# Kernel optimization log

Hardware: AMD Instinct MI355X
Metric: run time of the kernel (lower is better)

The kernel has to match this reference:

```python
import jax, jax.numpy as jnp
import numpy as np

K_NEIGHBORS = 3  # self.K in DSVDD


def setup_inputs() -> dict:
    key = jax.random.key(0)
    k1, k2 = jax.random.split(key)
    B, N, C = 16, 3136, 112   # batch, h*w patches, descriptor channels
    M = 3136                  # memory-bank size
    phi_p = jax.random.normal(k1, (B, N, C), dtype=jnp.float32)
    C_bank = jax.random.normal(k2, (C, M), dtype=jnp.float32)
    return {"phi_p": phi_p, "C_bank": C_bank, "h": 56}


def reference(phi_p, C_bank, h):
    # squared distances via ||phi||^2 + ||c||^2 - 2 phi.c  -> (B, N, M)
    features = jnp.sum(phi_p * phi_p, axis=2, keepdims=True)        # (B, N, 1)
    centers = jnp.sum(C_bank * C_bank, axis=0, keepdims=True)       # (1, M)
    f_c = 2.0 * jnp.einsum('bnc,cm->bnm', phi_p, C_bank)            # (B, N, M)
    dist = jnp.sqrt(features + centers - f_c)                        # (B, N, M)
    # K smallest distances (ascending, like torch.topk(largest=False))
    neg_topk, _ = jax.lax.top_k(-dist, K_NEIGHBORS)                  # (B, N, K)
    dist_k = -neg_topk
    # softmin over K, take weight of the nearest neighbor times its distance
    softmin0 = jax.nn.softmax(-dist_k, axis=-1)[:, :, 0]             # (B, N)
    score = softmin0 * dist_k[:, :, 0]                               # (B, N)
    B, N = score.shape
    w = N // h
    return score.reshape(B, 1, h, w)  # b c h w with c=1
```

## Files before the change

### kernel.cpp

```cpp
#include <hip/hip_runtime.h>
#include <stdint.h>


typedef short s16x8 __attribute__((ext_vector_type(8)));
typedef float fx4 __attribute__((ext_vector_type(4)));

#define M_TOT 3136
#define CC 112
#define NROWS 50176
#define N_TILES_TOT 50

__device__ __forceinline__ unsigned short f2bf(float x) {
  unsigned u = __float_as_uint(x);
  u += 0x7fffu + ((u >> 16) & 1u);
  return (unsigned short)(u >> 16);
}

#define INSERT3(T0, T1, T2, V)                                  \
  do {                                                          \
    const float _a0 = (T0), _a1 = (T1), _v = (V);               \
    (T0) = fmaxf(_a0, _v);                                      \
    (T1) = __builtin_amdgcn_fmed3f(_a0, _a1, _v);               \
    (T2) = __builtin_amdgcn_fmed3f(_a1, (T2), _v);              \
  } while (0)

__global__ __launch_bounds__(256) void dsvdd_prep(const float* __restrict__ Cb,
                                                  unsigned char* __restrict__ CT2) {
  const int tile = blockIdx.x;
  __shared__ float partial[256];
  __shared__ float c2s[64];
  const int tm = threadIdx.x & 63;
  const int seg = threadIdx.x >> 6;
  const int m = tile * 64 + tm;
  float ss = 0.f;
  if (m < M_TOT) {
    for (int k = seg * 28; k < seg * 28 + 28; ++k) {
      const float x = Cb[(size_t)k * M_TOT + m];
      ss += x * x;
    }
  }
  partial[threadIdx.x] = ss;
  __syncthreads();
  if (seg == 0) {
    const float c2 = partial[tm] + partial[64 + tm] + partial[128 + tm] + partial[192 + tm];
    c2s[tm] = (m < M_TOT) ? (-0.125f * c2) : -2500.0f;
  }
  __syncthreads();
#pragma unroll
  for (int it = 0; it < 4; ++it) {
    const int s = it * 256 + threadIdx.x;
    const int f = s >> 8;
    const int ks = (s >> 6) & 3;
    const int l = s & 63;
    const int mloc = f * 16 + (l & 15);
    const int mm = tile * 64 + mloc;
    const bool mv = (mm < M_TOT);
    const int k0 = ks * 32 + (l >> 4) * 8;
    float v[8];
#pragma unroll
    for (int j = 0; j < 8; ++j) {
      const int k = k0 + j;
      float x = 0.f;
      if (k < CC) x = mv ? Cb[(size_t)k * M_TOT + mm] : 0.f;
      else if (k < 116) x = c2s[mloc];
      v[j] = x;
    }
    uint4 pk;
    pk.x = (unsigned)f2bf(v[0]) | ((unsigned)f2bf(v[1]) << 16);
    pk.y = (unsigned)f2bf(v[2]) | ((unsigned)f2bf(v[3]) << 16);
    pk.z = (unsigned)f2bf(v[4]) | ((unsigned)f2bf(v[5]) << 16);
    pk.w = (unsigned)f2bf(v[6]) | ((unsigned)f2bf(v[7]) << 16);
    *(uint4*)(CT2 + (size_t)tile * 16384 + (size_t)s * 16) = pk;
  }
}

__global__ __launch_bounds__(256, 2) void dsvdd_stage1(const float* __restrict__ phi,
                                                       const unsigned char* __restrict__ CT2,
                                                       float* __restrict__ part,
                                                       float* __restrict__ featg, int nT) {
  __shared__ float mg[128][8];

  const int t = threadIdx.x;
  const int lane = t & 63;
  const int w = t >> 6;
  const int g = w >> 1;
  const int h = w & 1;
  const int cq = lane & 15;
  const int kq = lane >> 4;
  const int c = blockIdx.y;
  const int tile0 = c * nT;
  const long rowBase = (long)blockIdx.x * 128;
  const bool needF = (c == 0);

  s16x8 bg[4][4];
  float ssr[4];
#pragma unroll
  for (int pf = 0; pf < 4; ++pf) {
    ssr[pf] = 0.f;
    const float* rp = phi + (size_t)(rowBase + g * 64 + pf * 16 + cq) * CC;
#pragma unroll
    for (int ks = 0; ks < 4; ++ks) {
      const int k0 = ks * 32 + kq * 8;
      s16x8 v;
      if (k0 <= 104) {
        const float4 a = *(const float4*)(rp + k0);
        const float4 b = *(const float4*)(rp + k0 + 4);
        if (needF) {
          ssr[pf] += a.x * a.x + a.y * a.y + a.z * a.z + a.w * a.w;
          ssr[pf] += b.x * b.x + b.y * b.y + b.z * b.z + b.w * b.w;
        }
        v[0] = (short)f2bf(a.x); v[1] = (short)f2bf(a.y);
        v[2] = (short)f2bf(a.z); v[3] = (short)f2bf(a.w);
        v[4] = (short)f2bf(b.x); v[5] = (short)f2bf(b.y);
        v[6] = (short)f2bf(b.z); v[7] = (short)f2bf(b.w);
      } else if (k0 == 112) {
        v[0] = v[1] = v[2] = v[3] = (short)0x3f80;
        v[4] = v[5] = v[6] = v[7] = 0;
      } else {
        v = (s16x8)0;
      }
      bg[ks][pf] = v;
    }
    if (needF) {
      ssr[pf] += __shfl_xor(ssr[pf], 16);
      ssr[pf] += __shfl_xor(ssr[pf], 32);
    }
  }
  if (needF && kq == 0) {
#pragma unroll
    for (int pf = 0; pf < 4; ++pf)
      featg[rowBase + g * 64 + pf * 16 + cq] = ssr[pf];
  }

  float t0[4], t1[4], t2[4];
#pragma unroll
  for (int pf = 0; pf < 4; ++pf) t0[pf] = t1[pf] = t2[pf] = -3.0e38f;

  const unsigned char* ap = CT2 + (size_t)(h * 2) * 4096 + (size_t)lane * 16;
  s16x8 afA[8], afB[8];

#define LOADAF(DST, TIDX)                                                     \
  do {                                                                        \
    const unsigned char* _p = ap + (size_t)(TIDX)*16384;                      \
    _Pragma("unroll") for (int mf = 0; mf < 2; ++mf)                          \
        _Pragma("unroll") for (int ks = 0; ks < 4; ++ks)                      \
            DST[mf * 4 + ks] = *(const s16x8*)(_p + mf * 4096 + ks * 1024);   \
  } while (0)

#define COMPUTE(SRC)                                                          \
  do {                                                                        \
    const fx4 _zz = {0.f, 0.f, 0.f, 0.f};                                     \
    _Pragma("unroll") for (int mf = 0; mf < 2; ++mf) {                        \
      fx4 acc[4];                                                             \
      _Pragma("unroll") for (int ks = 0; ks < 4; ++ks)                        \
          _Pragma("unroll") for (int pf = 0; pf < 4; ++pf)                    \
              acc[pf] = __builtin_amdgcn_mfma_f32_16x16x32_bf16(              \
                  SRC[mf * 4 + ks], bg[ks][pf], (ks == 0) ? _zz : acc[pf],    \
                  0, 0, 0);                                                   \
      _Pragma("unroll") for (int pf = 0; pf < 4; ++pf)                        \
          _Pragma("unroll") for (int rg = 0; rg < 4; ++rg)                    \
              INSERT3(t0[pf], t1[pf], t2[pf], acc[pf][rg]);                   \
    }                                                                         \
  } while (0)

  LOADAF(afA, tile0);
  int tt = 0;
  while (tt + 2 < nT) {
    LOADAF(afB, tile0 + tt + 1);
    COMPUTE(afA);
    LOADAF(afA, tile0 + tt + 2);
    COMPUTE(afB);
    tt += 2;
  }
  if (tt + 1 < nT) {
    LOADAF(afB, tile0 + tt + 1);
    COMPUTE(afA);
    COMPUTE(afB);
  } else {
    COMPUTE(afA);
  }
#undef LOADAF
#undef COMPUTE

#pragma unroll
  for (int pf = 0; pf < 4; ++pf) {
#pragma unroll
    for (int off = 16; off < 64; off <<= 1) {
      const float b0 = __shfl_xor(t0[pf], off);
      const float b1 = __shfl_xor(t1[pf], off);
      const float b2 = __shfl_xor(t2[pf], off);
      INSERT3(t0[pf], t1[pf], t2[pf], b0);
      INSERT3(t0[pf], t1[pf], t2[pf], b1);
      INSERT3(t0[pf], t1[pf], t2[pf], b2);
    }
  }
  if (kq == 0) {
#pragma unroll
    for (int pf = 0; pf < 4; ++pf) {
      const int row = g * 64 + pf * 16 + cq;
      mg[row][h * 3 + 0] = t0[pf];
      mg[row][h * 3 + 1] = t1[pf];
      mg[row][h * 3 + 2] = t2[pf];
    }
  }
  __syncthreads();
  if (t < 128) {
    float s0 = mg[t][0], s1 = mg[t][1], s2 = mg[t][2];
    INSERT3(s0, s1, s2, mg[t][3]);
    INSERT3(s0, s1, s2, mg[t][4]);
    INSERT3(s0, s1, s2, mg[t][5]);
    float* dst = part + ((size_t)c * NROWS + rowBase + t) * 3;
    dst[0] = s0; dst[1] = s1; dst[2] = s2;
  }
}

__global__ __launch_bounds__(256) void dsvdd_stage2(const float* __restrict__ part,
                                                    const float* __restrict__ featg,
                                                    float* __restrict__ out, int S) {
  const int row = blockIdx.x * 256 + threadIdx.x;
  if (row >= NROWS) return;
  float s0 = -3.0e38f, s1 = -3.0e38f, s2 = -3.0e38f;
  for (int c = 0; c < S; ++c) {
    const float* p = part + ((size_t)c * NROWS + row) * 3;
    INSERT3(s0, s1, s2, p[0]);
    INSERT3(s0, s1, s2, p[1]);
    INSERT3(s0, s1, s2, p[2]);
  }
  const float feat = featg[row];
  const float d0 = sqrtf(fmaxf(feat - 2.f * s0, 0.f));
  const float d1 = sqrtf(fmaxf(feat - 2.f * s1, 0.f));
  const float d2 = sqrtf(fmaxf(feat - 2.f * s2, 0.f));
  const float w0 = 1.0f / (1.0f + __expf(d0 - d1) + __expf(d0 - d2));
  out[row] = w0 * d0;
}

extern "C" void kernel_launch(void* const* d_in, const int* in_sizes, int n_in,
                              void* d_out, int out_size, void* d_ws, size_t ws_size,
                              hipStream_t stream) {
  (void)in_sizes; (void)n_in; (void)out_size;
  const float* phi = (const float*)d_in[0];
  const float* Cb = (const float*)d_in[1];
  float* out = (float*)d_out;
  unsigned char* CT2 = (unsigned char*)d_ws;
  float* featg = (float*)((unsigned char*)d_ws + 819200);
  float* partp = (float*)((unsigned char*)d_ws + 819200 + 200704);
  const size_t base = 819200 + 200704;
  int S = 1;
  if (ws_size >= base + (size_t)5 * NROWS * 12) S = 5;
  else if (ws_size >= base + (size_t)2 * NROWS * 12) S = 2;
  const int nT = N_TILES_TOT / S;
  dsvdd_prep<<<50, 256, 0, stream>>>(Cb, CT2);
  dsvdd_stage1<<<dim3(392, S), 256, 0, stream>>>(phi, CT2, partp, featg, nT);
  dsvdd_stage2<<<196, 256, 0, stream>>>(partp, featg, out, S);
}
```

Measured before the change: 64.28 us.

## Stage phi rows through shared memory and raise occupancy target to three blocks

Each block now loads its 128 phi rows cooperatively with contiguous per-thread reads, converts them to bf16 once, and writes them into a 32KB shared buffer in MFMA fragment order. Waves then read their B fragments from LDS. Before, each wave converted its own rows from global memory and both wave halves duplicated that work. Launch bounds are also raised to 3 blocks per CU, which cuts the register budget and may cause spills given the large fragment arrays.

```diff
diff --git a/kernel.cpp b/kernel.cpp
--- a/kernel.cpp
+++ b/kernel.cpp
@@ -74,11 +74,12 @@
   }
 }
 
-__global__ __launch_bounds__(256, 2) void dsvdd_stage1(const float* __restrict__ phi,
+__global__ __launch_bounds__(256, 3) void dsvdd_stage1(const float* __restrict__ phi,
                                                        const unsigned char* __restrict__ CT2,
                                                        float* __restrict__ part,
                                                        float* __restrict__ featg, int nT) {
-  __shared__ float mg[128][8];
+  __shared__ __align__(16) unsigned char phiF[32768];
+  float(*const mg)[8] = (float(*)[8])phiF;
 
   const int t = threadIdx.x;
   const int lane = t & 63;
@@ -92,45 +93,47 @@
   const long rowBase = (long)blockIdx.x * 128;
   const bool needF = (c == 0);
 
+  {
+    const int r = t >> 1;
+    const int h2 = t & 1;
+    const float* src = phi + (size_t)(rowBase + r) * CC + h2 * 56;
+    unsigned char* const base = phiF + (((r >> 4) * 4) * 1024);
+    const int pcq = r & 15;
+    float ss = 0.f;
+#pragma unroll
+    for (int j = 0; j < 7; ++j) {
+      const int k0 = h2 * 56 + j * 8;
+      const int ks = k0 >> 5;
+      const int kqw = (k0 >> 3) & 3;
+      const float4 a = *(const float4*)(src + j * 8);
+      const float4 b = *(const float4*)(src + j * 8 + 4);
+      ss += a.x * a.x + a.y * a.y + a.z * a.z + a.w * a.w;
+      ss += b.x * b.x + b.y * b.y + b.z * b.z + b.w * b.w;
+      uint4 pk;
+      pk.x = (unsigned)f2bf(a.x) | ((unsigned)f2bf(a.y) << 16);
+      pk.y = (unsigned)f2bf(a.z) | ((unsigned)f2bf(a.w) << 16);
+      pk.z = (unsigned)f2bf(b.x) | ((unsigned)f2bf(b.y) << 16);
+      pk.w = (unsigned)f2bf(b.z) | ((unsigned)f2bf(b.w) << 16);
+      *(uint4*)(base + ks * 1024 + (kqw * 16 + pcq) * 16) = pk;
+    }
+    {
+      uint4 pk;
+      if (h2 == 0) { pk.x = 0x3f803f80u; pk.y = 0x3f803f80u; pk.z = 0u; pk.w = 0u; }
+      else { pk.x = pk.y = pk.z = pk.w = 0u; }
+      *(uint4*)(base + 3 * 1024 + ((2 + h2) * 16 + pcq) * 16) = pk;
+    }
+    ss += __shfl_xor(ss, 1);
+    if (needF && h2 == 0) featg[rowBase + r] = ss;
+  }
+  __syncthreads();
+
   s16x8 bg[4][4];
-  float ssr[4];
-#pragma unroll
-  for (int pf = 0; pf < 4; ++pf) {
-    ssr[pf] = 0.f;
-    const float* rp = phi + (size_t)(rowBase + g * 64 + pf * 16 + cq) * CC;
-#pragma unroll
-    for (int ks = 0; ks < 4; ++ks) {
-      const int k0 = ks * 32 + kq * 8;
-      s16x8 v;
-      if (k0 <= 104) {
-        const float4 a = *(const float4*)(rp + k0);
-        const float4 b = *(const float4*)(rp + k0 + 4);
-        if (needF) {
-          ssr[pf] += a.x * a.x + a.y * a.y + a.z * a.z + a.w * a.w;
-          ssr[pf] += b.x * b.x + b.y * b.y + b.z * b.z + b.w * b.w;
-        }
-        v[0] = (short)f2bf(a.x); v[1] = (short)f2bf(a.y);
-        v[2] = (short)f2bf(a.z); v[3] = (short)f2bf(a.w);
-        v[4] = (short)f2bf(b.x); v[5] = (short)f2bf(b.y);
-        v[6] = (short)f2bf(b.z); v[7] = (short)f2bf(b.w);
-      } else if (k0 == 112) {
-        v[0] = v[1] = v[2] = v[3] = (short)0x3f80;
-        v[4] = v[5] = v[6] = v[7] = 0;
-      } else {
-        v = (s16x8)0;
-      }
-      bg[ks][pf] = v;
-    }
-    if (needF) {
-      ssr[pf] += __shfl_xor(ssr[pf], 16);
-      ssr[pf] += __shfl_xor(ssr[pf], 32);
-    }
-  }
-  if (needF && kq == 0) {
+#pragma unroll
+  for (int ks = 0; ks < 4; ++ks)
 #pragma unroll
     for (int pf = 0; pf < 4; ++pf)
-      featg[rowBase + g * 64 + pf * 16 + cq] = ssr[pf];
-  }
+      bg[ks][pf] = *(const s16x8*)(phiF + (((g * 4 + pf) * 4 + ks) * 64 + lane) * 16);
+  __syncthreads();
 
   float t0[4], t1[4], t2[4];
 #pragma unroll
```

Result: no change. 63.45 us (-1.3%).
